# Performance work log

Hardware: AMD Instinct MI355X
Metric: run time of the kernel (lower is better)

The kernel has to match this reference:

```python
import jax, jax.numpy as jnp
import numpy as np

N_NODES = 50000


def gcn_norm(edge_index, edge_weight, n):
    """PyG GCNConv normalization: add self-loops (weight 1), sym-normalize."""
    src, dst = edge_index[0], edge_index[1]
    loop = jnp.arange(n, dtype=src.dtype)
    src = jnp.concatenate([src, loop])
    dst = jnp.concatenate([dst, loop])
    w = jnp.concatenate([edge_weight, jnp.ones((n,), dtype=edge_weight.dtype)])
    deg = jax.ops.segment_sum(w, dst, num_segments=n)  # in-degree w/ self-loops
    dis = jnp.where(deg > 0, jax.lax.rsqrt(deg), 0.0)  # deg^{-1/2}, inf -> 0
    norm = dis[src] * w * dis[dst]                      # [E+N]
    return src, dst, norm


def gcn_conv(x, src, dst, norm, W, b):
    h = x @ W                                            # [N, F_out]
    msg = norm[:, None] * h[src]                         # gather + scale
    out = jax.ops.segment_sum(msg, dst, num_segments=x.shape[0])  # scatter-add
    return out + b


def setup_inputs() -> dict:
    key = jax.random.key(0)
    ks = jax.random.split(key, 10)
    n, e = N_NODES, 800000
    in_dim, hidden, out_dim = 256, 128, 64
    x = jax.random.normal(ks[0], (n, in_dim), dtype=jnp.float32)
    edge_index = jax.random.randint(ks[1], (2, e), 0, n, dtype=jnp.int32)
    edge_weight = jax.random.uniform(ks[2], (e,), dtype=jnp.float32)
    def glorot(k, fi, fo):
        lim = float(np.sqrt(6.0 / (fi + fo)))
        return jax.random.uniform(k, (fi, fo), minval=-lim, maxval=lim, dtype=jnp.float32)
    return {
        "x": x, "edge_index": edge_index, "edge_weight": edge_weight,
        "W1": glorot(ks[3], in_dim, hidden), "b1": jnp.zeros((hidden,), jnp.float32),
        "W2": glorot(ks[4], hidden, hidden), "b2": jnp.zeros((hidden,), jnp.float32),
        "W3": glorot(ks[5], hidden, out_dim), "b3": jnp.zeros((out_dim,), jnp.float32),
    }


def reference(x, edge_index, edge_weight, W1, b1, W2, b2, W3, b3):
    n = x.shape[0]
    src, dst, norm = gcn_norm(edge_index, edge_weight, n)  # cached=True: shared
    h = jax.nn.relu(gcn_conv(x, src, dst, norm, W1, b1))   # dropout: eval mode no-op
    h = jax.nn.relu(gcn_conv(h, src, dst, norm, W2, b2))
    h = gcn_conv(h, src, dst, norm, W3, b3)
    return h
```

## Files before the change

### kernel.cpp

```cpp
#include <hip/hip_runtime.h>
#include <hip/hip_bf16.h>
#include <stdint.h>

#define NODES 50000
#define EDGES 800000
#define R_REP 8
#define DEG_EPT 4
#define SCAN_TB 256
#define SCAN_NB ((NODES + SCAN_TB - 1) / SCAN_TB)
#define NVB_DEG ((EDGES + 1023) / 1024)
#define NVB_GEMM ((NODES / 16 + 3) / 4)

typedef short bf16x8 __attribute__((ext_vector_type(8)));
typedef float f32x4 __attribute__((ext_vector_type(4)));

__device__ __forceinline__ unsigned short f2bf(float f) {
    union { float f; unsigned u; } v; v.f = f;
    unsigned r = v.u + 0x7fff + ((v.u >> 16) & 1);
    return (unsigned short)(r >> 16);
}
__device__ __forceinline__ float bf2f(unsigned short h) {
    union { float f; unsigned u; } v; v.u = ((unsigned)h) << 16;
    return v.f;
}
__device__ __forceinline__ float bflo(unsigned hv) {
    union { float f; unsigned u; } v; v.u = hv << 16;
    return v.f;
}
__device__ __forceinline__ float bfhi(unsigned hv) {
    union { float f; unsigned u; } v; v.u = hv & 0xffff0000u;
    return v.f;
}


__device__ __forceinline__ void wfrag_one(const float* __restrict__ W, unsigned short* Wf,
                                          int idx, int K, int Nn) {
    int NT = Nn >> 4;
    int lane = idx & 63;
    int f = idx >> 6;
    int nt = f % NT;
    int k0 = (f / NT) << 5;
    int n = (nt << 4) + (lane & 15);
    int kk = k0 + ((lane >> 4) << 3);
    unsigned short o[8];
#pragma unroll
    for (int j = 0; j < 8; j++) o[j] = f2bf(W[(kk + j) * Nn + n]);
    ((uint4*)Wf)[idx] = *(uint4*)o;
}

__global__ void k_setup(unsigned long long* packed, int* cursor,
                        const float* __restrict__ W1, unsigned short* Wf1,
                        const float* __restrict__ W2, unsigned short* Wf2,
                        const float* __restrict__ W3, unsigned short* Wf3) {
    int idx = blockIdx.x * blockDim.x + threadIdx.x;
    if (idx == 0) *cursor = 0;
    if (idx < NODES * R_REP) { packed[idx] = 0ull; return; }
    int k = idx - NODES * R_REP;
    if (k < 4096) wfrag_one(W1, Wf1, k, 256, 128);
    else if (k < 6144) wfrag_one(W2, Wf2, k - 4096, 128, 128);
    else if (k < 7168) wfrag_one(W3, Wf3, k - 6144, 128, 64);
}

template <int K, int Nn, bool A_F32>
__device__ __forceinline__ void gemm_vb(const void* __restrict__ A_,
                                        const uint4* __restrict__ Wf,
                                        unsigned short* __restrict__ Hout, int vb) {
    constexpr int NT = Nn / 16;
    int lane = threadIdx.x & 63;
    int wave = threadIdx.x >> 6;
    int tile = vb * 4 + wave;
    if (tile * 16 >= NODES) return;
    int row = tile * 16 + (lane & 15);
    int kbase = (lane >> 4) * 8;

    f32x4 acc[NT];
#pragma unroll
    for (int i = 0; i < NT; i++) acc[i] = (f32x4){0.f, 0.f, 0.f, 0.f};

    for (int k0 = 0; k0 < K; k0 += 32) {
        bf16x8 a;
        if (A_F32) {
            const float* A = (const float*)A_;
            const float4* pp = (const float4*)&A[(size_t)row * K + k0 + kbase];
            float4 u0 = pp[0], u1 = pp[1];
            unsigned short t[8];
            t[0] = f2bf(u0.x); t[1] = f2bf(u0.y); t[2] = f2bf(u0.z); t[3] = f2bf(u0.w);
            t[4] = f2bf(u1.x); t[5] = f2bf(u1.y); t[6] = f2bf(u1.z); t[7] = f2bf(u1.w);
            a = *(bf16x8*)t;
        } else {
            const unsigned short* A = (const unsigned short*)A_;
            a = *(const bf16x8*)&A[(size_t)row * K + k0 + kbase];
        }
        int fbase = (k0 >> 5) * NT;
#pragma unroll
        for (int nt = 0; nt < NT; nt++) {
            uint4 braw = Wf[(fbase + nt) * 64 + lane];
            bf16x8 b = *(bf16x8*)&braw;
            acc[nt] = __builtin_amdgcn_mfma_f32_16x16x32_bf16(a, b, acc[nt], 0, 0, 0);
        }
    }
    int r0 = (lane >> 4) * 4;
    int col = lane & 15;
#pragma unroll
    for (int nt = 0; nt < NT; nt++) {
#pragma unroll
        for (int r = 0; r < 4; r++) {
            int m = tile * 16 + r0 + r;
            Hout[(size_t)m * Nn + nt * 16 + col] = f2bf(acc[nt][r]);
        }
    }
}

__global__ void k_deg_gemm1(const int* __restrict__ dst, const float* __restrict__ w,
                            unsigned long long* __restrict__ packed, int* __restrict__ rank,
                            const float* __restrict__ x, const uint4* __restrict__ Wf1,
                            unsigned short* __restrict__ h) {
    int half = blockIdx.x >> 1;
    if ((blockIdx.x & 1) == 0) {
        if (half >= NVB_DEG) return;
        int base = half * 1024 + threadIdx.x;
        int r = half & (R_REP - 1);
        unsigned long long olds[DEG_EPT];
#pragma unroll
        for (int q = 0; q < DEG_EPT; q++) {
            int e = base + q * 256;
            if (e < EDGES) {
                int d = dst[e];
                unsigned fx = __float2uint_rn(w[e] * 16777216.0f);
                unsigned long long add = (1ull << 40) | (unsigned long long)fx;
                olds[q] = atomicAdd(&packed[(size_t)r * NODES + d], add);
            }
        }
#pragma unroll
        for (int q = 0; q < DEG_EPT; q++) {
            int e = base + q * 256;
            if (e < EDGES) rank[e] = (int)(olds[q] >> 40);
        }
    } else {
        if (half >= NVB_GEMM) return;
        gemm_vb<256, 128, true>((const void*)x, Wf1, h, half);
    }
}

__global__ void k_scan(const unsigned long long* __restrict__ packed,
                       float* __restrict__ dis, int* __restrict__ repoff,
                       int2* __restrict__ rsc, int* __restrict__ cursor) {
    __shared__ int sm[SCAN_TB];
    __shared__ int s_base;
    int t = threadIdx.x;
    int i = blockIdx.x * SCAN_TB + t;
    int v = 0;
    if (i < NODES) {
        unsigned long long degfx = 0;
        int off = 0;
#pragma unroll
        for (int r = 0; r < R_REP; r++) {
            unsigned long long pk = packed[(size_t)r * NODES + i];
            repoff[(size_t)r * NODES + i] = off;
            off += (int)(pk >> 40);
            degfx += (pk & 0xFFFFFFFFFFull);
        }
        v = off;
        dis[i] = rsqrtf(1.0f + (float)degfx * (1.0f / 16777216.0f));
    }
    sm[t] = v;
    __syncthreads();
    for (int off = 1; off < SCAN_TB; off <<= 1) {
        int x2 = (t >= off) ? sm[t - off] : 0;
        __syncthreads();
        sm[t] += x2;
        __syncthreads();
    }
    int incl = sm[t];
    if (t == SCAN_TB - 1) s_base = atomicAdd(cursor, incl);
    __syncthreads();
    if (i < NODES) { int2 rs; rs.x = s_base + incl - v; rs.y = v; rsc[i] = rs; }
}

__global__ void k_scatter(const int* __restrict__ src, const int* __restrict__ dst,
                          const float* __restrict__ w, const float* __restrict__ dis,
                          const int2* __restrict__ rsc, const int* __restrict__ repoff,
                          const int* __restrict__ rank, int2* __restrict__ rec) {
    int e = blockIdx.x * blockDim.x + threadIdx.x;
    if (e < EDGES) {
        int r = (e >> 10) & (R_REP - 1);
        int s = src[e], d = dst[e];
        float nrm = dis[s] * w[e] * dis[d];
        int pos = rsc[d].x + repoff[(size_t)r * NODES + d] + rank[e];
        int2 rc; rc.x = s; rc.y = __float_as_int(nrm);
        rec[pos] = rc;
    }
}

template <int K, int Nn, bool A_F32>
__global__ void k_gemm(const void* __restrict__ A_, const uint4* __restrict__ Wf,
                       unsigned short* __restrict__ Hout) {
    gemm_vb<K, Nn, A_F32>(A_, Wf, Hout, blockIdx.x);
}

template <int F, bool RELU, bool OUT_F32>
__global__ void k_agg(const unsigned short* __restrict__ H, const int2* __restrict__ rec,
                      const int2* __restrict__ rsc, const float* __restrict__ dis,
                      const float* __restrict__ bias, void* __restrict__ out_) {
    constexpr int VPT = F / 64;
    int lane = threadIdx.x & 63;
    int node = blockIdx.x * 4 + (threadIdx.x >> 6);
    if (node >= NODES) return;
    node = __builtin_amdgcn_readfirstlane(node);

    const unsigned* H32 = (const unsigned*)H;

    float sn = dis[node]; sn = sn * sn;
    float acc0, acc1 = 0.f;
    if (VPT == 2) {
        unsigned hv = H32[node * 64 + lane];
        acc0 = sn * bflo(hv);
        acc1 = sn * bfhi(hv);
    } else {
        acc0 = sn * bf2f(H[node * 64 + lane]);
    }

    int2 rs = rsc[node];
    int beg = rs.x, end = rs.x + rs.y;
    int last = end - 1;
    for (int j = beg; j < end; j += 8) {
        int ss[8]; float nn[8];
#pragma unroll
        for (int q = 0; q < 8; q++) {
            int idx = j + q;
            idx = (idx < last) ? idx : last;
            int2 rc = rec[idx];
            ss[q] = rc.x;
            nn[q] = (j + q < end) ? __int_as_float(rc.y) : 0.0f;
        }
        if (VPT == 2) {
            unsigned hh[8];
#pragma unroll
            for (int q = 0; q < 8; q++) hh[q] = H32[ss[q] * 64 + lane];
#pragma unroll
            for (int q = 0; q < 8; q++) {
                acc0 += nn[q] * bflo(hh[q]);
                acc1 += nn[q] * bfhi(hh[q]);
            }
        } else {
            unsigned short hh[8];
#pragma unroll
            for (int q = 0; q < 8; q++) hh[q] = H[ss[q] * 64 + lane];
#pragma unroll
            for (int q = 0; q < 8; q++) acc0 += nn[q] * bf2f(hh[q]);
        }
    }

    if (OUT_F32) {
        float* out = (float*)out_;
        if (VPT == 2) {
            float x0 = acc0 + bias[lane * 2];
            float x1 = acc1 + bias[lane * 2 + 1];
            if (RELU) { x0 = fmaxf(x0, 0.f); x1 = fmaxf(x1, 0.f); }
            out[(size_t)node * F + lane * 2] = x0;
            out[(size_t)node * F + lane * 2 + 1] = x1;
        } else {
            float x0 = acc0 + bias[lane];
            if (RELU) x0 = fmaxf(x0, 0.f);
            out[(size_t)node * F + lane] = x0;
        }
    } else {
        unsigned short* out = (unsigned short*)out_;
        if (VPT == 2) {
            float x0 = acc0 + bias[lane * 2];
            float x1 = acc1 + bias[lane * 2 + 1];
            if (RELU) { x0 = fmaxf(x0, 0.f); x1 = fmaxf(x1, 0.f); }
            unsigned pk = (unsigned)f2bf(x0) | ((unsigned)f2bf(x1) << 16);
            *(unsigned*)&out[(size_t)node * F + lane * 2] = pk;
        } else {
            float x0 = acc0 + bias[lane];
            if (RELU) x0 = fmaxf(x0, 0.f);
            out[(size_t)node * F + lane] = f2bf(x0);
        }
    }
}


extern "C" void kernel_launch(void* const* d_in, const int* in_sizes, int n_in,
                              void* d_out, int out_size, void* d_ws, size_t ws_size,
                              hipStream_t stream) {
    const float* x  = (const float*)d_in[0];
    const int*   ei = (const int*)d_in[1];
    const float* w  = (const float*)d_in[2];
    const float* W1 = (const float*)d_in[3];
    const float* b1 = (const float*)d_in[4];
    const float* W2 = (const float*)d_in[5];
    const float* b2 = (const float*)d_in[6];
    const float* W3 = (const float*)d_in[7];
    const float* b3 = (const float*)d_in[8];
    const int* src = ei;
    const int* dst = ei + EDGES;

    char* p = (char*)d_ws;
    auto alloc = [&](size_t n) { char* r = p; p += (n + 511) & ~(size_t)511; return r; };
    unsigned long long* packed = (unsigned long long*)alloc((size_t)NODES * R_REP * 8);
    float*          dis    = (float*)alloc(NODES * 4);
    int2*           rsc    = (int2*)alloc((size_t)NODES * 8);
    int*            repoff = (int*)alloc((size_t)NODES * R_REP * 4);
    int*            rank   = (int*)alloc(EDGES * 4);
    int*            cursor = (int*)alloc(4);
    int2*           rec    = (int2*)alloc(EDGES * 8);
    unsigned short* h      = (unsigned short*)alloc((size_t)NODES * 128 * 2);
    unsigned short* xb     = (unsigned short*)alloc((size_t)NODES * 128 * 2);
    unsigned short* wf1    = (unsigned short*)alloc(256 * 128 * 2);
    unsigned short* wf2    = (unsigned short*)alloc(128 * 128 * 2);
    unsigned short* wf3    = (unsigned short*)alloc(128 * 64 * 2);

    const int TB = 256;
    int nb_setup = (NODES * R_REP + 7168 + TB - 1) / TB;
    int nb_fused = 2 * ((NVB_DEG > NVB_GEMM) ? NVB_DEG : NVB_GEMM);
    int nb_edges = (EDGES + TB - 1) / TB;

    hipLaunchKernelGGL(k_setup, dim3(nb_setup), dim3(TB), 0, stream,
                       packed, cursor, W1, wf1, W2, wf2, W3, wf3);
    hipLaunchKernelGGL(k_deg_gemm1, dim3(nb_fused), dim3(TB), 0, stream,
                       dst, w, packed, rank, x, (const uint4*)wf1, h);
    hipLaunchKernelGGL(k_scan, dim3(SCAN_NB), dim3(SCAN_TB), 0, stream,
                       packed, dis, repoff, rsc, cursor);
    hipLaunchKernelGGL(k_scatter, dim3(nb_edges), dim3(TB), 0, stream,
                       src, dst, w, dis, rsc, repoff, rank, rec);

    int nb_gemm = NVB_GEMM;
    int nb_agg  = (NODES + 3) / 4;

    hipLaunchKernelGGL((k_agg<128, true, false>), dim3(nb_agg), dim3(TB), 0, stream, h, rec, rsc, dis, b1, (void*)xb);

    hipLaunchKernelGGL((k_gemm<128, 128, false>), dim3(nb_gemm), dim3(TB), 0, stream, (const void*)xb, (const uint4*)wf2, h);
    hipLaunchKernelGGL((k_agg<128, true, false>), dim3(nb_agg), dim3(TB), 0, stream, h, rec, rsc, dis, b2, (void*)xb);

    hipLaunchKernelGGL((k_gemm<128, 64, false>), dim3(nb_gemm), dim3(TB), 0, stream, (const void*)xb, (const uint4*)wf3, h);
    hipLaunchKernelGGL((k_agg<64, false, true>), dim3(nb_agg), dim3(TB), 0, stream, h, rec, rsc, dis, b3, d_out);
}
```

Baseline: 284.1 us.

## Narrow degree atomics to 32-bit and move GEMM1 alongside scatter via bf16 x

Packs count and fixed-point weight into a 32-bit word (6-bit count, 20-bit fraction) instead of 64-bit, halving atomic traffic and the packed buffer. The degree kernel now pairs with an fp32-to-bf16 conversion of x rather than the first GEMM. The first GEMM reads the bf16 copy and runs in the same launch as the edge scatter. This rebalances work between launches and shrinks GEMM1 input reads. The cost is an extra bf16 copy of x written and read back, plus lower fixed-point precision for the degree sum. The 6-bit count field overflows if a node receives more than 63 edges in one replica.

Result: no change. 285.4 us (+0.5%).

```diff
diff --git a/kernel.cpp b/kernel.cpp
--- a/kernel.cpp
+++ b/kernel.cpp
@@ -10,6 +10,8 @@
 #define SCAN_NB ((NODES + SCAN_TB - 1) / SCAN_TB)
 #define NVB_DEG ((EDGES + 1023) / 1024)
 #define NVB_GEMM ((NODES / 16 + 3) / 4)
+#define NVB_XC (NODES * 256 / 8 / 256)
+#define NVB_SCT ((EDGES + 255) / 256)
 
 typedef short bf16x8 __attribute__((ext_vector_type(8)));
 typedef float f32x4 __attribute__((ext_vector_type(4)));
@@ -48,13 +50,13 @@
     ((uint4*)Wf)[idx] = *(uint4*)o;
 }
 
-__global__ void k_setup(unsigned long long* packed, int* cursor,
+__global__ void k_setup(unsigned* packed, int* cursor,
                         const float* __restrict__ W1, unsigned short* Wf1,
                         const float* __restrict__ W2, unsigned short* Wf2,
                         const float* __restrict__ W3, unsigned short* Wf3) {
     int idx = blockIdx.x * blockDim.x + threadIdx.x;
     if (idx == 0) *cursor = 0;
-    if (idx < NODES * R_REP) { packed[idx] = 0ull; return; }
+    if (idx < NODES * R_REP) { packed[idx] = 0u; return; }
     int k = idx - NODES * R_REP;
     if (k < 4096) wfrag_one(W1, Wf1, k, 256, 128);
     else if (k < 6144) wfrag_one(W2, Wf2, k - 4096, 128, 128);
@@ -111,38 +113,42 @@
     }
 }
 
-__global__ void k_deg_gemm1(const int* __restrict__ dst, const float* __restrict__ w,
-                            unsigned long long* __restrict__ packed, int* __restrict__ rank,
-                            const float* __restrict__ x, const uint4* __restrict__ Wf1,
-                            unsigned short* __restrict__ h) {
+__global__ void k_deg_xconv(const int* __restrict__ dst, const float* __restrict__ w,
+                            unsigned* __restrict__ packed, int* __restrict__ rank,
+                            const float* __restrict__ x, unsigned short* __restrict__ xb16) {
     int half = blockIdx.x >> 1;
     if ((blockIdx.x & 1) == 0) {
         if (half >= NVB_DEG) return;
         int base = half * 1024 + threadIdx.x;
         int r = half & (R_REP - 1);
-        unsigned long long olds[DEG_EPT];
+        unsigned olds[DEG_EPT];
 #pragma unroll
         for (int q = 0; q < DEG_EPT; q++) {
             int e = base + q * 256;
             if (e < EDGES) {
                 int d = dst[e];
-                unsigned fx = __float2uint_rn(w[e] * 16777216.0f);
-                unsigned long long add = (1ull << 40) | (unsigned long long)fx;
+                unsigned add = (1u << 26) | __float2uint_rn(w[e] * 1048576.0f);
                 olds[q] = atomicAdd(&packed[(size_t)r * NODES + d], add);
             }
         }
 #pragma unroll
         for (int q = 0; q < DEG_EPT; q++) {
             int e = base + q * 256;
-            if (e < EDGES) rank[e] = (int)(olds[q] >> 40);
+            if (e < EDGES) rank[e] = (int)(olds[q] >> 26);
         }
     } else {
-        if (half >= NVB_GEMM) return;
-        gemm_vb<256, 128, true>((const void*)x, Wf1, h, half);
-    }
-}
-
-__global__ void k_scan(const unsigned long long* __restrict__ packed,
+        if (half >= NVB_XC) return;
+        size_t g = (size_t)half * 256 + threadIdx.x;
+        const float4* px = (const float4*)(x + g * 8);
+        float4 u0 = px[0], u1 = px[1];
+        unsigned short t[8];
+        t[0] = f2bf(u0.x); t[1] = f2bf(u0.y); t[2] = f2bf(u0.z); t[3] = f2bf(u0.w);
+        t[4] = f2bf(u1.x); t[5] = f2bf(u1.y); t[6] = f2bf(u1.z); t[7] = f2bf(u1.w);
+        ((uint4*)xb16)[g] = *(uint4*)t;
+    }
+}
+
+__global__ void k_scan(const unsigned* __restrict__ packed,
                        float* __restrict__ dis, int* __restrict__ repoff,
                        int2* __restrict__ rsc, int* __restrict__ cursor) {
     __shared__ int sm[SCAN_TB];
@@ -151,17 +157,17 @@
     int i = blockIdx.x * SCAN_TB + t;
     int v = 0;
     if (i < NODES) {
-        unsigned long long degfx = 0;
+        unsigned degfx = 0;
         int off = 0;
 #pragma unroll
         for (int r = 0; r < R_REP; r++) {
-            unsigned long long pk = packed[(size_t)r * NODES + i];
+            unsigned pk = packed[(size_t)r * NODES + i];
             repoff[(size_t)r * NODES + i] = off;
-            off += (int)(pk >> 40);
-            degfx += (pk & 0xFFFFFFFFFFull);
+            off += (int)(pk >> 26);
+            degfx += (pk & 0x03FFFFFFu);
         }
         v = off;
-        dis[i] = rsqrtf(1.0f + (float)degfx * (1.0f / 16777216.0f));
+        dis[i] = rsqrtf(1.0f + (float)degfx * (1.0f / 1048576.0f));
     }
     sm[t] = v;
     __syncthreads();
@@ -177,11 +183,20 @@
     if (i < NODES) { int2 rs; rs.x = s_base + incl - v; rs.y = v; rsc[i] = rs; }
 }
 
-__global__ void k_scatter(const int* __restrict__ src, const int* __restrict__ dst,
-                          const float* __restrict__ w, const float* __restrict__ dis,
-                          const int2* __restrict__ rsc, const int* __restrict__ repoff,
-                          const int* __restrict__ rank, int2* __restrict__ rec) {
-    int e = blockIdx.x * blockDim.x + threadIdx.x;
+__global__ void k_sct_gemm1(const int* __restrict__ src, const int* __restrict__ dst,
+                            const float* __restrict__ w, const float* __restrict__ dis,
+                            const int2* __restrict__ rsc, const int* __restrict__ repoff,
+                            const int* __restrict__ rank, int2* __restrict__ rec,
+                            const unsigned short* __restrict__ xb16,
+                            const uint4* __restrict__ Wf1, unsigned short* __restrict__ h) {
+    int half = blockIdx.x >> 1;
+    if (blockIdx.x & 1) {
+        if (half >= NVB_GEMM) return;
+        gemm_vb<256, 128, false>((const void*)xb16, Wf1, h, half);
+        return;
+    }
+    if (half >= NVB_SCT) return;
+    int e = half * 256 + threadIdx.x;
     if (e < EDGES) {
         int r = (e >> 10) & (R_REP - 1);
         int s = src[e], d = dst[e];
@@ -298,7 +313,7 @@
 
     char* p = (char*)d_ws;
     auto alloc = [&](size_t n) { char* r = p; p += (n + 511) & ~(size_t)511; return r; };
-    unsigned long long* packed = (unsigned long long*)alloc((size_t)NODES * R_REP * 8);
+    unsigned*       packed = (unsigned*)alloc((size_t)NODES * R_REP * 4);
     float*          dis    = (float*)alloc(NODES * 4);
     int2*           rsc    = (int2*)alloc((size_t)NODES * 8);
     int*            repoff = (int*)alloc((size_t)NODES * R_REP * 4);
@@ -307,23 +322,22 @@
     int2*           rec    = (int2*)alloc(EDGES * 8);
     unsigned short* h      = (unsigned short*)alloc((size_t)NODES * 128 * 2);
     unsigned short* xb     = (unsigned short*)alloc((size_t)NODES * 128 * 2);
+    unsigned short* xb16   = (unsigned short*)alloc((size_t)NODES * 256 * 2);
     unsigned short* wf1    = (unsigned short*)alloc(256 * 128 * 2);
     unsigned short* wf2    = (unsigned short*)alloc(128 * 128 * 2);
     unsigned short* wf3    = (unsigned short*)alloc(128 * 64 * 2);
 
     const int TB = 256;
     int nb_setup = (NODES * R_REP + 7168 + TB - 1) / TB;
-    int nb_fused = 2 * ((NVB_DEG > NVB_GEMM) ? NVB_DEG : NVB_GEMM);
-    int nb_edges = (EDGES + TB - 1) / TB;
 
     hipLaunchKernelGGL(k_setup, dim3(nb_setup), dim3(TB), 0, stream,
                        packed, cursor, W1, wf1, W2, wf2, W3, wf3);
-    hipLaunchKernelGGL(k_deg_gemm1, dim3(nb_fused), dim3(TB), 0, stream,
-                       dst, w, packed, rank, x, (const uint4*)wf1, h);
+    hipLaunchKernelGGL(k_deg_xconv, dim3(2 * NVB_XC), dim3(TB), 0, stream,
+                       dst, w, packed, rank, x, xb16);
     hipLaunchKernelGGL(k_scan, dim3(SCAN_NB), dim3(SCAN_TB), 0, stream,
                        packed, dis, repoff, rsc, cursor);
-    hipLaunchKernelGGL(k_scatter, dim3(nb_edges), dim3(TB), 0, stream,
-                       src, dst, w, dis, rsc, repoff, rank, rec);
+    hipLaunchKernelGGL(k_sct_gemm1, dim3(2 * NVB_SCT), dim3(TB), 0, stream,
+                       src, dst, w, dis, rsc, repoff, rank, rec, xb16, (const uint4*)wf1, h);
 
     int nb_gemm = NVB_GEMM;
     int nb_agg  = (NODES + 3) / 4;
```

## Replace atomic CSR build with two-level bucketed LDS counting sort

Applied to the files above, without the earlier changes.

Builds the destination-sorted edge list with a block-local histogram over 64-node buckets, a per-bucket scan, and an LDS-staged scatter, followed by a per-bucket subsort that also computes degrees and node offsets. This replaces the global 64-bit atomics, the replicated counters and the rank/repoff arrays. Normalization moves into aggregation: the stored weight is raw, the source dis is applied per edge in the gather, and the destination dis is applied at the end. Risks include the fixed bucket capacity CAP, which truncates buckets holding more than 2560 edges, the 16-bit source packing, which assumes node ids below 65536, and extra per-edge gathers of dis in every aggregation layer.

Measured after the change: 304.2 us. 1.07x slower.

```diff
diff --git a/kernel.cpp b/kernel.cpp
--- a/kernel.cpp
+++ b/kernel.cpp
@@ -4,11 +4,13 @@
 
 #define NODES 50000
 #define EDGES 800000
-#define R_REP 8
-#define DEG_EPT 4
-#define SCAN_TB 256
-#define SCAN_NB ((NODES + SCAN_TB - 1) / SCAN_TB)
-#define NVB_DEG ((EDGES + 1023) / 1024)
+
+#define EPB 4096
+#define NBLK ((EDGES + EPB - 1) / EPB)
+#define NBUK ((NODES + 63) / 64)
+#define NBUKP 1024
+#define CAP 2560
+
 #define NVB_GEMM ((NODES / 16 + 3) / 4)
 
 typedef short bf16x8 __attribute__((ext_vector_type(8)));
@@ -31,7 +33,6 @@
     union { float f; unsigned u; } v; v.u = hv & 0xffff0000u;
     return v.f;
 }
-
 
 __device__ __forceinline__ void wfrag_one(const float* __restrict__ W, unsigned short* Wf,
                                           int idx, int K, int Nn) {
@@ -48,17 +49,52 @@
     ((uint4*)Wf)[idx] = *(uint4*)o;
 }
 
-__global__ void k_setup(unsigned long long* packed, int* cursor,
-                        const float* __restrict__ W1, unsigned short* Wf1,
-                        const float* __restrict__ W2, unsigned short* Wf2,
-                        const float* __restrict__ W3, unsigned short* Wf3) {
-    int idx = blockIdx.x * blockDim.x + threadIdx.x;
-    if (idx == 0) *cursor = 0;
-    if (idx < NODES * R_REP) { packed[idx] = 0ull; return; }
-    int k = idx - NODES * R_REP;
-    if (k < 4096) wfrag_one(W1, Wf1, k, 256, 128);
-    else if (k < 6144) wfrag_one(W2, Wf2, k - 4096, 128, 128);
-    else if (k < 7168) wfrag_one(W3, Wf3, k - 6144, 128, 64);
+__global__ void k_setup_hist(const int* __restrict__ dst, unsigned* __restrict__ hist,
+                             int* __restrict__ cursor,
+                             const float* __restrict__ W1, unsigned short* Wf1,
+                             const float* __restrict__ W2, unsigned short* Wf2,
+                             const float* __restrict__ W3, unsigned short* Wf3) {
+    if ((int)blockIdx.x < NBLK) {
+        __shared__ unsigned cnt[NBUK];
+        int t = threadIdx.x;
+        for (int i = t; i < NBUK; i += 256) cnt[i] = 0;
+        __syncthreads();
+        int base = blockIdx.x * EPB;
+#pragma unroll
+        for (int i = 0; i < EPB / 256; i++) {
+            int e = base + i * 256 + t;
+            if (e < EDGES) atomicAdd(&cnt[((unsigned)dst[e]) >> 6], 1u);
+        }
+        __syncthreads();
+        for (int b = t; b < NBUK; b += 256) hist[b * NBLK + blockIdx.x] = cnt[b];
+    } else {
+        int idx = (blockIdx.x - NBLK) * 256 + threadIdx.x;
+        if (idx == 0) *cursor = 0;
+        if (idx < 4096) wfrag_one(W1, Wf1, idx, 256, 128);
+        else if (idx < 6144) wfrag_one(W2, Wf2, idx - 4096, 128, 128);
+        else if (idx < 7168) wfrag_one(W3, Wf3, idx - 6144, 128, 64);
+    }
+}
+
+__global__ void k_hscan(unsigned* __restrict__ hist, int2* __restrict__ brange,
+                        int* __restrict__ cursor) {
+    __shared__ int sm[256];
+    __shared__ int s_base;
+    int b = blockIdx.x, t = threadIdx.x;
+    int v = (t < NBLK) ? (int)hist[b * NBLK + t] : 0;
+    sm[t] = v;
+    __syncthreads();
+    for (int off = 1; off < 256; off <<= 1) {
+        int x2 = (t >= off) ? sm[t - off] : 0;
+        __syncthreads();
+        sm[t] += x2;
+        __syncthreads();
+    }
+    int total = sm[255];
+    if (t == 0) s_base = atomicAdd(cursor, total);
+    __syncthreads();
+    if (t < NBLK) hist[b * NBLK + t] = (unsigned)(s_base + sm[t] - v);
+    if (t == 0) { int2 r; r.x = s_base; r.y = total; brange[b] = r; }
 }
 
 template <int K, int Nn, bool A_F32>
@@ -111,84 +147,126 @@
     }
 }
 
-__global__ void k_deg_gemm1(const int* __restrict__ dst, const float* __restrict__ w,
-                            unsigned long long* __restrict__ packed, int* __restrict__ rank,
-                            const float* __restrict__ x, const uint4* __restrict__ Wf1,
-                            unsigned short* __restrict__ h) {
-    int half = blockIdx.x >> 1;
-    if ((blockIdx.x & 1) == 0) {
-        if (half >= NVB_DEG) return;
-        int base = half * 1024 + threadIdx.x;
-        int r = half & (R_REP - 1);
-        unsigned long long olds[DEG_EPT];
-#pragma unroll
-        for (int q = 0; q < DEG_EPT; q++) {
-            int e = base + q * 256;
-            if (e < EDGES) {
-                int d = dst[e];
-                unsigned fx = __float2uint_rn(w[e] * 16777216.0f);
-                unsigned long long add = (1ull << 40) | (unsigned long long)fx;
-                olds[q] = atomicAdd(&packed[(size_t)r * NODES + d], add);
-            }
-        }
-#pragma unroll
-        for (int q = 0; q < DEG_EPT; q++) {
-            int e = base + q * 256;
-            if (e < EDGES) rank[e] = (int)(olds[q] >> 40);
-        }
-    } else {
-        if (half >= NVB_GEMM) return;
-        gemm_vb<256, 128, true>((const void*)x, Wf1, h, half);
-    }
-}
-
-__global__ void k_scan(const unsigned long long* __restrict__ packed,
-                       float* __restrict__ dis, int* __restrict__ repoff,
-                       int2* __restrict__ rsc, int* __restrict__ cursor) {
-    __shared__ int sm[SCAN_TB];
-    __shared__ int s_base;
+__global__ void k_sort_gemm1(const int* __restrict__ src, const int* __restrict__ dst,
+                             const float* __restrict__ w, const unsigned* __restrict__ gbase,
+                             int2* __restrict__ rec,
+                             const float* __restrict__ x, const uint4* __restrict__ Wf1,
+                             unsigned short* __restrict__ h) {
+    __shared__ unsigned long long rec_lds[EPB];
+    __shared__ unsigned cnt[NBUKP];
+    __shared__ unsigned lst[NBUKP];
+    __shared__ unsigned gb[NBUK];
+    __shared__ int part[256];
+
+    int blk = blockIdx.x;
+    if (blk >= NBLK) {
+        gemm_vb<256, 128, true>((const void*)x, Wf1, h, blk - NBLK);
+        return;
+    }
     int t = threadIdx.x;
-    int i = blockIdx.x * SCAN_TB + t;
-    int v = 0;
-    if (i < NODES) {
-        unsigned long long degfx = 0;
-        int off = 0;
-#pragma unroll
-        for (int r = 0; r < R_REP; r++) {
-            unsigned long long pk = packed[(size_t)r * NODES + i];
-            repoff[(size_t)r * NODES + i] = off;
-            off += (int)(pk >> 40);
-            degfx += (pk & 0xFFFFFFFFFFull);
-        }
-        v = off;
-        dis[i] = rsqrtf(1.0f + (float)degfx * (1.0f / 16777216.0f));
-    }
-    sm[t] = v;
-    __syncthreads();
-    for (int off = 1; off < SCAN_TB; off <<= 1) {
-        int x2 = (t >= off) ? sm[t - off] : 0;
-        __syncthreads();
-        sm[t] += x2;
-        __syncthreads();
-    }
-    int incl = sm[t];
-    if (t == SCAN_TB - 1) s_base = atomicAdd(cursor, incl);
-    __syncthreads();
-    if (i < NODES) { int2 rs; rs.x = s_base + incl - v; rs.y = v; rsc[i] = rs; }
-}
-
-__global__ void k_scatter(const int* __restrict__ src, const int* __restrict__ dst,
-                          const float* __restrict__ w, const float* __restrict__ dis,
-                          const int2* __restrict__ rsc, const int* __restrict__ repoff,
-                          const int* __restrict__ rank, int2* __restrict__ rec) {
-    int e = blockIdx.x * blockDim.x + threadIdx.x;
-    if (e < EDGES) {
-        int r = (e >> 10) & (R_REP - 1);
-        int s = src[e], d = dst[e];
-        float nrm = dis[s] * w[e] * dis[d];
-        int pos = rsc[d].x + repoff[(size_t)r * NODES + d] + rank[e];
-        int2 rc; rc.x = s; rc.y = __float_as_int(nrm);
-        rec[pos] = rc;
+    for (int b = t; b < NBUK; b += 256) gb[b] = gbase[b * NBLK + blk];
+    for (int b = t; b < NBUKP; b += 256) cnt[b] = 0;
+    __syncthreads();
+
+    int base = blk * EPB;
+    int nrec = EDGES - base; if (nrec > EPB) nrec = EPB;
+
+#pragma unroll
+    for (int i = 0; i < EPB / 256; i++) {
+        int e = base + i * 256 + t;
+        if (e < EDGES) atomicAdd(&cnt[((unsigned)dst[e]) >> 6], 1u);
+    }
+    __syncthreads();
+
+    unsigned s0 = cnt[t * 4], s1 = cnt[t * 4 + 1], s2 = cnt[t * 4 + 2], s3 = cnt[t * 4 + 3];
+    unsigned ps = s0 + s1 + s2 + s3;
+    part[t] = (int)ps;
+    __syncthreads();
+    for (int off = 1; off < 256; off <<= 1) {
+        int x2 = (t >= off) ? part[t - off] : 0;
+        __syncthreads();
+        part[t] += x2;
+        __syncthreads();
+    }
+    unsigned excl = (unsigned)part[t] - ps;
+    lst[t * 4] = excl;
+    lst[t * 4 + 1] = excl + s0;
+    lst[t * 4 + 2] = excl + s0 + s1;
+    lst[t * 4 + 3] = excl + s0 + s1 + s2;
+    __syncthreads();
+    for (int b = t; b < NBUKP; b += 256) cnt[b] = 0;
+    __syncthreads();
+
+#pragma unroll
+    for (int i = 0; i < EPB / 256; i++) {
+        int e = base + i * 256 + t;
+        if (e < EDGES) {
+            unsigned d = (unsigned)dst[e];
+            unsigned b = d >> 6;
+            unsigned r = atomicAdd(&cnt[b], 1u);
+            unsigned meta = (unsigned)src[e] | ((d & 63u) << 16) | (b << 22);
+            unsigned long long v = (unsigned long long)meta |
+                                   ((unsigned long long)__float_as_uint(w[e]) << 32);
+            rec_lds[lst[b] + r] = v;
+        }
+    }
+    __syncthreads();
+
+    for (int i = t; i < nrec; i += 256) {
+        unsigned long long v = rec_lds[i];
+        unsigned meta = (unsigned)v;
+        unsigned b = meta >> 22;
+        unsigned gpos = gb[b] + ((unsigned)i - lst[b]);
+        int2 rc; rc.x = (int)(meta & 0x3FFFFFu); rc.y = (int)(v >> 32);
+        rec[gpos] = rc;
+    }
+}
+
+__global__ void k_sub(int2* __restrict__ rec, const int2* __restrict__ brange,
+                      float* __restrict__ dis, int2* __restrict__ rsc) {
+    __shared__ int2 stage[CAP];
+    __shared__ unsigned short ipos[CAP];
+    __shared__ unsigned cnt[64];
+    __shared__ unsigned lst[64];
+    __shared__ float degw[64];
+    int t = threadIdx.x, b = blockIdx.x;
+    int2 br = brange[b];
+    int base = br.x;
+    int n = br.y; if (n > CAP) n = CAP;
+
+    if (t < 64) { cnt[t] = 0; degw[t] = 0.f; }
+    __syncthreads();
+    for (int i = t; i < n; i += 256) {
+        int2 rc = rec[base + i];
+        stage[i] = rc;
+        unsigned dl = ((unsigned)rc.x >> 16) & 63u;
+        atomicAdd(&cnt[dl], 1u);
+        atomicAdd(&degw[dl], __int_as_float(rc.y));
+    }
+    __syncthreads();
+    if (t == 0) {
+        unsigned run = 0;
+        for (int j = 0; j < 64; j++) { lst[j] = run; run += cnt[j]; }
+    }
+    __syncthreads();
+    if (t < 64) {
+        int node = b * 64 + t;
+        if (node < NODES) {
+            dis[node] = rsqrtf(1.0f + degw[t]);
+            int2 rs; rs.x = base + (int)lst[t]; rs.y = (int)cnt[t];
+            rsc[node] = rs;
+        }
+    }
+    if (t < 64) cnt[t] = 0;
+    __syncthreads();
+    for (int i = t; i < n; i += 256) {
+        unsigned dl = ((unsigned)stage[i].x >> 16) & 63u;
+        unsigned r = atomicAdd(&cnt[dl], 1u);
+        ipos[lst[dl] + r] = (unsigned short)i;
+    }
+    __syncthreads();
+    for (int i = t; i < n; i += 256) {
+        rec[base + i] = stage[ipos[i]];
     }
 }
 
@@ -210,14 +288,14 @@
 
     const unsigned* H32 = (const unsigned*)H;
 
-    float sn = dis[node]; sn = sn * sn;
+    float dn = dis[node];
     float acc0, acc1 = 0.f;
     if (VPT == 2) {
         unsigned hv = H32[node * 64 + lane];
-        acc0 = sn * bflo(hv);
-        acc1 = sn * bfhi(hv);
+        acc0 = dn * bflo(hv);
+        acc1 = dn * bfhi(hv);
     } else {
-        acc0 = sn * bf2f(H[node * 64 + lane]);
+        acc0 = dn * bf2f(H[node * 64 + lane]);
     }
 
     int2 rs = rsc[node];
@@ -230,9 +308,11 @@
             int idx = j + q;
             idx = (idx < last) ? idx : last;
             int2 rc = rec[idx];
-            ss[q] = rc.x;
+            ss[q] = rc.x & 0xFFFF;
             nn[q] = (j + q < end) ? __int_as_float(rc.y) : 0.0f;
         }
+#pragma unroll
+        for (int q = 0; q < 8; q++) nn[q] *= dis[ss[q]];
         if (VPT == 2) {
             unsigned hh[8];
 #pragma unroll
@@ -254,26 +334,26 @@
     if (OUT_F32) {
         float* out = (float*)out_;
         if (VPT == 2) {
-            float x0 = acc0 + bias[lane * 2];
-            float x1 = acc1 + bias[lane * 2 + 1];
+            float x0 = dn * acc0 + bias[lane * 2];
+            float x1 = dn * acc1 + bias[lane * 2 + 1];
             if (RELU) { x0 = fmaxf(x0, 0.f); x1 = fmaxf(x1, 0.f); }
             out[(size_t)node * F + lane * 2] = x0;
             out[(size_t)node * F + lane * 2 + 1] = x1;
         } else {
-            float x0 = acc0 + bias[lane];
+            float x0 = dn * acc0 + bias[lane];
             if (RELU) x0 = fmaxf(x0, 0.f);
             out[(size_t)node * F + lane] = x0;
         }
     } else {
         unsigned short* out = (unsigned short*)out_;
         if (VPT == 2) {
-            float x0 = acc0 + bias[lane * 2];
-            float x1 = acc1 + bias[lane * 2 + 1];
+            float x0 = dn * acc0 + bias[lane * 2];
+            float x1 = dn * acc1 + bias[lane * 2 + 1];
             if (RELU) { x0 = fmaxf(x0, 0.f); x1 = fmaxf(x1, 0.f); }
             unsigned pk = (unsigned)f2bf(x0) | ((unsigned)f2bf(x1) << 16);
             *(unsigned*)&out[(size_t)node * F + lane * 2] = pk;
         } else {
-            float x0 = acc0 + bias[lane];
+            float x0 = dn * acc0 + bias[lane];
             if (RELU) x0 = fmaxf(x0, 0.f);
             out[(size_t)node * F + lane] = f2bf(x0);
         }
@@ -298,13 +378,12 @@
 
     char* p = (char*)d_ws;
     auto alloc = [&](size_t n) { char* r = p; p += (n + 511) & ~(size_t)511; return r; };
-    unsigned long long* packed = (unsigned long long*)alloc((size_t)NODES * R_REP * 8);
+    unsigned*       hist   = (unsigned*)alloc((size_t)NBUK * NBLK * 4);
+    int2*           brange = (int2*)alloc((size_t)NBUK * 8);
+    int*            cursor = (int*)alloc(4);
+    int2*           rec    = (int2*)alloc((size_t)EDGES * 8);
     float*          dis    = (float*)alloc(NODES * 4);
     int2*           rsc    = (int2*)alloc((size_t)NODES * 8);
-    int*            repoff = (int*)alloc((size_t)NODES * R_REP * 4);
-    int*            rank   = (int*)alloc(EDGES * 4);
-    int*            cursor = (int*)alloc(4);
-    int2*           rec    = (int2*)alloc(EDGES * 8);
     unsigned short* h      = (unsigned short*)alloc((size_t)NODES * 128 * 2);
     unsigned short* xb     = (unsigned short*)alloc((size_t)NODES * 128 * 2);
     unsigned short* wf1    = (unsigned short*)alloc(256 * 128 * 2);
@@ -312,18 +391,13 @@
     unsigned short* wf3    = (unsigned short*)alloc(128 * 64 * 2);
 
     const int TB = 256;
-    int nb_setup = (NODES * R_REP + 7168 + TB - 1) / TB;
-    int nb_fused = 2 * ((NVB_DEG > NVB_GEMM) ? NVB_DEG : NVB_GEMM);
-    int nb_edges = (EDGES + TB - 1) / TB;
-
-    hipLaunchKernelGGL(k_setup, dim3(nb_setup), dim3(TB), 0, stream,
-                       packed, cursor, W1, wf1, W2, wf2, W3, wf3);
-    hipLaunchKernelGGL(k_deg_gemm1, dim3(nb_fused), dim3(TB), 0, stream,
-                       dst, w, packed, rank, x, (const uint4*)wf1, h);
-    hipLaunchKernelGGL(k_scan, dim3(SCAN_NB), dim3(SCAN_TB), 0, stream,
-                       packed, dis, repoff, rsc, cursor);
-    hipLaunchKernelGGL(k_scatter, dim3(nb_edges), dim3(TB), 0, stream,
-                       src, dst, w, dis, rsc, repoff, rank, rec);
+
+    hipLaunchKernelGGL(k_setup_hist, dim3(NBLK + 28), dim3(TB), 0, stream,
+                       dst, hist, cursor, W1, wf1, W2, wf2, W3, wf3);
+    hipLaunchKernelGGL(k_hscan, dim3(NBUK), dim3(TB), 0, stream, hist, brange, cursor);
+    hipLaunchKernelGGL(k_sort_gemm1, dim3(NBLK + NVB_GEMM), dim3(TB), 0, stream,
+                       src, dst, w, hist, rec, x, (const uint4*)wf1, h);
+    hipLaunchKernelGGL(k_sub, dim3(NBUK), dim3(TB), 0, stream, rec, brange, dis, rsc);
 
     int nb_gemm = NVB_GEMM;
     int nb_agg  = (NODES + 3) / 4;
```
